# Kernel tuning notes

Measured on AMD Instinct MI355X. Metric: run time of the kernel, lower is better.

Reference implementation:

```python
import jax, jax.numpy as jnp
from jax import lax
import numpy as np

B, H, W, C = 16, 56, 56, 256
IMAGE_SHAPE = (224, 224)
SIGMA = 4.0


def gaussian_blur(x, sigma):
    # cv2.GaussianBlur with ksize = 2*round(4*sigma)+1, BORDER_REFLECT_101 (= jnp 'reflect')
    r = int(round(4 * sigma))
    k = 2 * r + 1
    i = jnp.arange(k, dtype=x.dtype) - r
    g = jnp.exp(-(i * i) / (2.0 * sigma * sigma))
    g = g / jnp.sum(g)
    xp = jnp.pad(x, ((0, 0), (r, r), (r, r), (0, 0)), mode='reflect')
    dn = ('NHWC', 'HWIO', 'NHWC')
    x = lax.conv_general_dilated(xp, g.reshape(k, 1, 1, 1), (1, 1), 'VALID', dimension_numbers=dn)
    x = lax.conv_general_dilated(x, g.reshape(1, k, 1, 1), (1, 1), 'VALID', dimension_numbers=dn)
    return x


def setup_inputs() -> dict:
    key = jax.random.key(0)
    k1, k2, k3 = jax.random.split(key, 3)
    inputs = jax.random.normal(k1, (B, H, W, C), dtype=jnp.float32)
    mean = jax.random.normal(k2, (H * W, C), dtype=jnp.float32)
    # build a PSD inverse-covariance per pixel so the Mahalanobis quadratic form is >= 0
    A = jax.random.normal(k3, (H * W, C, C), dtype=jnp.float32)
    cvar_inv = jnp.einsum('pij,pkj->pik', A, A) / C + 0.1 * jnp.eye(C, dtype=jnp.float32)[None]
    return {"inputs": inputs, "mean": mean, "cvar_inv": cvar_inv}


def reference(inputs, mean, cvar_inv):
    b = inputs.shape[0]
    h, w, c = inputs.shape[1:]
    feature = inputs.reshape(b, h * w, c)
    # per-pixel Mahalanobis distance, batched over all pixels at once
    diff = feature - mean[None]                              # [b, hw, c]
    quad = jnp.einsum('bpc,pcd,bpd->bp', diff, cvar_inv, diff)
    mask = jnp.sqrt(jnp.maximum(quad, 0.0))                  # [b, hw]
    mask = mask.reshape(b, h, w, 1)
    mask = jax.image.resize(mask, (b, *IMAGE_SHAPE, 1), method='bilinear')
    if SIGMA > 0:
        mask = gaussian_blur(mask, SIGMA)
    score = jnp.max(mask, axis=(1, 2, 3))[:, None]           # [b, 1]
    return score, mask
```

## Files before the change

kernel.cpp:

```cpp
#include <hip/hip_runtime.h>
#include <math.h>

#define HWPIX 3136
#define CH    256
#define NB    16
#define IMG   224

__global__ void mahal_kernel(const float* __restrict__ inputs,
                             const float* __restrict__ mean,
                             const float* __restrict__ cvar,
                             float* __restrict__ mask_small)
{
    const int p    = blockIdx.x;
    const int tid  = threadIdx.x;
    const int lane = tid & 63;
    const int w    = tid >> 6;

    __shared__ float sdiff[CH * 20];
    __shared__ float sred[4][16];

    const float* mrow_mean = mean + (size_t)p * CH;

    {
        float mv = mrow_mean[tid];
        #pragma unroll
        for (int b = 0; b < NB; ++b) {
            float v = inputs[((size_t)b * HWPIX + p) * CH + tid] - mv;
            sdiff[tid * 20 + b] = v;
        }
    }
    __syncthreads();

    const float* M = cvar + (size_t)p * CH * CH;
    const int c4 = lane * 4;

    float4 acc[NB];
    #pragma unroll
    for (int b = 0; b < NB; ++b) acc[b] = make_float4(0.f, 0.f, 0.f, 0.f);

    #pragma unroll 2
    for (int k = 0; k < 64; ++k) {
        const int d = (w << 6) + k;
        const float4 m = *reinterpret_cast<const float4*>(M + (size_t)d * CH + c4);
        const float4* sdv = reinterpret_cast<const float4*>(&sdiff[d * 20]);
        const float4 dv0 = sdv[0];
        const float4 dv1 = sdv[1];
        const float4 dv2 = sdv[2];
        const float4 dv3 = sdv[3];
        const float dvals[16] = {dv0.x, dv0.y, dv0.z, dv0.w,
                                 dv1.x, dv1.y, dv1.z, dv1.w,
                                 dv2.x, dv2.y, dv2.z, dv2.w,
                                 dv3.x, dv3.y, dv3.z, dv3.w};
        #pragma unroll
        for (int b = 0; b < NB; ++b) {
            const float s = dvals[b];
            acc[b].x = fmaf(m.x, s, acc[b].x);
            acc[b].y = fmaf(m.y, s, acc[b].y);
            acc[b].z = fmaf(m.z, s, acc[b].z);
            acc[b].w = fmaf(m.w, s, acc[b].w);
        }
    }

    const float4 mn = *reinterpret_cast<const float4*>(mrow_mean + c4);
    float q[NB];
    #pragma unroll
    for (int b = 0; b < NB; ++b) {
        const float4 f = *reinterpret_cast<const float4*>(inputs + ((size_t)b * HWPIX + p) * CH + c4);
        const float4 df = make_float4(f.x - mn.x, f.y - mn.y, f.z - mn.z, f.w - mn.w);
        q[b] = acc[b].x * df.x + acc[b].y * df.y + acc[b].z * df.z + acc[b].w * df.w;
    }

    #pragma unroll
    for (int b = 0; b < NB; ++b) {
        float v = q[b];
        for (int off = 32; off > 0; off >>= 1) v += __shfl_xor(v, off, 64);
        if (lane == 0) sred[w][b] = v;
    }
    __syncthreads();
    if (tid < NB) {
        const float s = sred[0][tid] + sred[1][tid] + sred[2][tid] + sred[3][tid];
        mask_small[(size_t)tid * HWPIX + p] = sqrtf(fmaxf(s, 0.0f));
    }
}

__global__ void resize_kernel(const float* __restrict__ small_, float* __restrict__ out)
{
    const int idx = blockIdx.x * 256 + threadIdx.x;
    const int b   = idx / (IMG * IMG);
    const int rem = idx % (IMG * IMG);
    const int oy  = rem / IMG;
    const int ox  = rem % IMG;

    float fy = oy * 0.25f - 0.375f;
    float fx = ox * 0.25f - 0.375f;
    fy = fminf(fmaxf(fy, 0.0f), 55.0f);
    fx = fminf(fmaxf(fx, 0.0f), 55.0f);
    int iy0 = min((int)fy, 54);
    int ix0 = min((int)fx, 54);
    const float wy = fy - iy0;
    const float wx = fx - ix0;

    const float* s = small_ + (size_t)b * HWPIX;
    const float v00 = s[iy0 * 56 + ix0];
    const float v01 = s[iy0 * 56 + ix0 + 1];
    const float v10 = s[(iy0 + 1) * 56 + ix0];
    const float v11 = s[(iy0 + 1) * 56 + ix0 + 1];
    const float v0 = v00 + wx * (v01 - v00);
    const float v1 = v10 + wx * (v11 - v10);
    out[idx] = v0 + wy * (v1 - v0);
}

__device__ __forceinline__ void setup_gauss(float* g, float* norm, int tid)
{
    if (tid < 33) {
        const int i = tid - 16;
        g[tid] = expf((float)(-(i * i)) / 32.0f);
    }
    __syncthreads();
    if (tid == 0) {
        float s = 0.f;
        for (int i = 0; i < 33; ++i) s += g[i];
        *norm = 1.0f / s;
    }
    __syncthreads();
}

__global__ void blurh_kernel(const float* __restrict__ in, float* __restrict__ out)
{
    __shared__ float g[33];
    __shared__ float norm;
    const int tid = threadIdx.x;
    setup_gauss(g, &norm, tid);

    const int idx = blockIdx.x * 256 + tid;
    const int b   = idx / (IMG * IMG);
    const int rem = idx % (IMG * IMG);
    const int y   = rem / IMG;
    const int x   = rem % IMG;

    const float* src = in + (size_t)b * IMG * IMG;
    float acc = 0.f;
    #pragma unroll
    for (int i = -16; i <= 16; ++i) {
        int yy = y + i;
        yy = yy < 0 ? -yy : (yy > 223 ? 446 - yy : yy);
        acc += g[i + 16] * src[yy * IMG + x];
    }
    out[idx] = acc * norm;
}

__global__ void blurw_kernel(const float* __restrict__ in, float* __restrict__ mask_out,
                             float* __restrict__ score)
{
    __shared__ float g[33];
    __shared__ float norm;
    __shared__ float m4[4];
    const int tid = threadIdx.x;
    setup_gauss(g, &norm, tid);

    const int idx = blockIdx.x * 256 + tid;
    const int b   = idx / (IMG * IMG);
    const int rem = idx % (IMG * IMG);
    const int y   = rem / IMG;
    const int x   = rem % IMG;

    const float* src = in + (size_t)b * IMG * IMG;
    float acc = 0.f;
    #pragma unroll
    for (int i = -16; i <= 16; ++i) {
        int xx = x + i;
        xx = xx < 0 ? -xx : (xx > 223 ? 446 - xx : xx);
        acc += g[i + 16] * src[y * IMG + xx];
    }
    acc *= norm;
    mask_out[idx] = acc;

    float v = acc;
    for (int off = 32; off > 0; off >>= 1) v = fmaxf(v, __shfl_xor(v, off, 64));
    const int lane = tid & 63;
    const int w    = tid >> 6;
    if (lane == 0) m4[w] = v;
    __syncthreads();
    if (tid == 0) {
        const float mm = fmaxf(fmaxf(m4[0], m4[1]), fmaxf(m4[2], m4[3]));
        atomicMax(reinterpret_cast<int*>(score) + b, __float_as_int(mm));
    }
}

__global__ void init_score(float* __restrict__ score)
{
    if (threadIdx.x < NB) score[threadIdx.x] = 0.0f;
}

extern "C" void kernel_launch(void* const* d_in, const int* in_sizes, int n_in,
                              void* d_out, int out_size, void* d_ws, size_t ws_size,
                              hipStream_t stream)
{
    const float* inputs = (const float*)d_in[0];
    const float* mean   = (const float*)d_in[1];
    const float* cvar   = (const float*)d_in[2];

    float* score    = (float*)d_out;
    float* mask_out = (float*)d_out + NB;

    char* ws = (char*)d_ws;
    float* mask_small = (float*)ws;
    float* resized    = (float*)(ws + (size_t)NB * HWPIX * 4);
    float* tmp        = (float*)(ws + (size_t)NB * HWPIX * 4
                                    + (size_t)NB * IMG * IMG * 4);

    mahal_kernel <<<HWPIX, 256, 0, stream>>>(inputs, mean, cvar, mask_small);
    resize_kernel<<<(NB * IMG * IMG) / 256, 256, 0, stream>>>(mask_small, resized);
    blurh_kernel <<<(NB * IMG * IMG) / 256, 256, 0, stream>>>(resized, tmp);
    init_score   <<<1, 64, 0, stream>>>(score);
    blurw_kernel <<<(NB * IMG * IMG) / 256, 256, 0, stream>>>(tmp, mask_out, score);
}
```

Measured before the change: 1.130 ms.

## Fuse resize and separable blur into one tiled kernel; software-pipeline cvar loads

Replaces the separate resize, vertical blur and horizontal blur kernels with one tail kernel per (4-row strip, batch). Each block recomputes the bilinear resize for its halo rows into shared memory, applies both blur passes there, and reduces the max, so the full-size intermediates no longer make a global round-trip. The Mahalanobis kernel now prefetches cvar rows four ahead in registers and declares launch bounds. Gaussian weights become precomputed constants. The cost is redundant halo resize work (36 rows computed per 4 output rows) and extra register pressure in the main kernel.

```diff
diff --git a/kernel.cpp b/kernel.cpp
--- a/kernel.cpp
+++ b/kernel.cpp
@@ -5,11 +5,44 @@
 #define CH    256
 #define NB    16
 #define IMG   224
-
-__global__ void mahal_kernel(const float* __restrict__ inputs,
-                             const float* __restrict__ mean,
-                             const float* __restrict__ cvar,
-                             float* __restrict__ mask_small)
+#define TY    4
+
+__constant__ float GW[33] = {
+    3.3458800e-05f, 8.8152100e-05f, 2.1817847e-04f, 5.0728021e-04f,
+    1.1080013e-03f, 2.2734742e-03f, 4.3822299e-03f, 7.9351934e-03f,
+    1.3498218e-02f, 2.1570092e-02f, 3.2380543e-02f, 4.5663884e-02f,
+    6.0494818e-02f, 7.5287016e-02f, 8.8019438e-02f, 9.6670425e-02f,
+    9.9739093e-02f, 9.6670425e-02f, 8.8019438e-02f, 7.5287016e-02f,
+    6.0494818e-02f, 4.5663884e-02f, 3.2380543e-02f, 2.1570092e-02f,
+    1.3498218e-02f, 7.9351934e-03f, 4.3822299e-03f, 2.2734742e-03f,
+    1.1080013e-03f, 5.0728021e-04f, 2.1817847e-04f, 8.8152100e-05f,
+    3.3458800e-05f
+};
+
+
+#define MAHAL_ROW(D, MVEC)                                                       \
+    {                                                                            \
+        const float4* sdv = reinterpret_cast<const float4*>(&sdiff[(D) * 20]);   \
+        const float4 dv0 = sdv[0], dv1 = sdv[1], dv2 = sdv[2], dv3 = sdv[3];     \
+        const float dsv[16] = {dv0.x, dv0.y, dv0.z, dv0.w,                       \
+                               dv1.x, dv1.y, dv1.z, dv1.w,                       \
+                               dv2.x, dv2.y, dv2.z, dv2.w,                       \
+                               dv3.x, dv3.y, dv3.z, dv3.w};                      \
+        _Pragma("unroll")                                                        \
+        for (int b = 0; b < NB; ++b) {                                           \
+            const float s = dsv[b];                                              \
+            acc[b].x = fmaf((MVEC).x, s, acc[b].x);                              \
+            acc[b].y = fmaf((MVEC).y, s, acc[b].y);                              \
+            acc[b].z = fmaf((MVEC).z, s, acc[b].z);                              \
+            acc[b].w = fmaf((MVEC).w, s, acc[b].w);                              \
+        }                                                                        \
+    }
+
+__global__ __launch_bounds__(256, 4)
+void mahal_kernel(const float* __restrict__ inputs,
+                  const float* __restrict__ mean,
+                  const float* __restrict__ cvar,
+                  float* __restrict__ mask_small)
 {
     const int p    = blockIdx.x;
     const int tid  = threadIdx.x;
@@ -22,43 +55,39 @@
     const float* mrow_mean = mean + (size_t)p * CH;
 
     {
-        float mv = mrow_mean[tid];
+        const float mv = mrow_mean[tid];
         #pragma unroll
         for (int b = 0; b < NB; ++b) {
-            float v = inputs[((size_t)b * HWPIX + p) * CH + tid] - mv;
-            sdiff[tid * 20 + b] = v;
+            sdiff[tid * 20 + b] = inputs[((size_t)b * HWPIX + p) * CH + tid] - mv;
         }
     }
     __syncthreads();
 
-    const float* M = cvar + (size_t)p * CH * CH;
-    const int c4 = lane * 4;
+    const int c4   = lane * 4;
+    const int row0 = w << 6;
+    const float* Mb = cvar + (size_t)p * CH * CH + (size_t)row0 * CH + c4;
 
     float4 acc[NB];
     #pragma unroll
     for (int b = 0; b < NB; ++b) acc[b] = make_float4(0.f, 0.f, 0.f, 0.f);
 
-    #pragma unroll 2
-    for (int k = 0; k < 64; ++k) {
-        const int d = (w << 6) + k;
-        const float4 m = *reinterpret_cast<const float4*>(M + (size_t)d * CH + c4);
-        const float4* sdv = reinterpret_cast<const float4*>(&sdiff[d * 20]);
-        const float4 dv0 = sdv[0];
-        const float4 dv1 = sdv[1];
-        const float4 dv2 = sdv[2];
-        const float4 dv3 = sdv[3];
-        const float dvals[16] = {dv0.x, dv0.y, dv0.z, dv0.w,
-                                 dv1.x, dv1.y, dv1.z, dv1.w,
-                                 dv2.x, dv2.y, dv2.z, dv2.w,
-                                 dv3.x, dv3.y, dv3.z, dv3.w};
-        #pragma unroll
-        for (int b = 0; b < NB; ++b) {
-            const float s = dvals[b];
-            acc[b].x = fmaf(m.x, s, acc[b].x);
-            acc[b].y = fmaf(m.y, s, acc[b].y);
-            acc[b].z = fmaf(m.z, s, acc[b].z);
-            acc[b].w = fmaf(m.w, s, acc[b].w);
+    float4 mr[4];
+    #pragma unroll
+    for (int i = 0; i < 4; ++i)
+        mr[i] = *reinterpret_cast<const float4*>(Mb + i * CH);
+
+    #pragma unroll 3
+    for (int kk = 0; kk < 60; kk += 4) {
+        #pragma unroll
+        for (int i = 0; i < 4; ++i) {
+            const float4 m = mr[i];
+            mr[i] = *reinterpret_cast<const float4*>(Mb + (kk + 4 + i) * CH);
+            MAHAL_ROW(row0 + kk + i, m)
         }
+    }
+    #pragma unroll
+    for (int i = 0; i < 4; ++i) {
+        MAHAL_ROW(row0 + 60 + i, mr[i])
     }
 
     const float4 mn = *reinterpret_cast<const float4*>(mrow_mean + c4);
@@ -83,103 +112,72 @@
     }
 }
 
-__global__ void resize_kernel(const float* __restrict__ small_, float* __restrict__ out)
-{
-    const int idx = blockIdx.x * 256 + threadIdx.x;
-    const int b   = idx / (IMG * IMG);
-    const int rem = idx % (IMG * IMG);
-    const int oy  = rem / IMG;
-    const int ox  = rem % IMG;
-
-    float fy = oy * 0.25f - 0.375f;
-    float fx = ox * 0.25f - 0.375f;
-    fy = fminf(fmaxf(fy, 0.0f), 55.0f);
-    fx = fminf(fmaxf(fx, 0.0f), 55.0f);
-    int iy0 = min((int)fy, 54);
-    int ix0 = min((int)fx, 54);
-    const float wy = fy - iy0;
-    const float wx = fx - ix0;
+__global__ void tail_kernel(const float* __restrict__ small_,
+                            float* __restrict__ mask_out,
+                            float* __restrict__ score)
+{
+    const int b   = blockIdx.y;
+    const int y0  = blockIdx.x * TY;
+    const int tid = threadIdx.x;
+
+    __shared__ float S[TY + 32][IMG];
+    __shared__ float Hb[TY][IMG];
+    __shared__ float m4[4];
 
     const float* s = small_ + (size_t)b * HWPIX;
-    const float v00 = s[iy0 * 56 + ix0];
-    const float v01 = s[iy0 * 56 + ix0 + 1];
-    const float v10 = s[(iy0 + 1) * 56 + ix0];
-    const float v11 = s[(iy0 + 1) * 56 + ix0 + 1];
-    const float v0 = v00 + wx * (v01 - v00);
-    const float v1 = v10 + wx * (v11 - v10);
-    out[idx] = v0 + wy * (v1 - v0);
-}
-
-__device__ __forceinline__ void setup_gauss(float* g, float* norm, int tid)
-{
-    if (tid < 33) {
-        const int i = tid - 16;
-        g[tid] = expf((float)(-(i * i)) / 32.0f);
-    }
-    __syncthreads();
-    if (tid == 0) {
-        float s = 0.f;
-        for (int i = 0; i < 33; ++i) s += g[i];
-        *norm = 1.0f / s;
-    }
-    __syncthreads();
-}
-
-__global__ void blurh_kernel(const float* __restrict__ in, float* __restrict__ out)
-{
-    __shared__ float g[33];
-    __shared__ float norm;
-    const int tid = threadIdx.x;
-    setup_gauss(g, &norm, tid);
-
-    const int idx = blockIdx.x * 256 + tid;
-    const int b   = idx / (IMG * IMG);
-    const int rem = idx % (IMG * IMG);
-    const int y   = rem / IMG;
-    const int x   = rem % IMG;
-
-    const float* src = in + (size_t)b * IMG * IMG;
-    float acc = 0.f;
-    #pragma unroll
-    for (int i = -16; i <= 16; ++i) {
-        int yy = y + i;
-        yy = yy < 0 ? -yy : (yy > 223 ? 446 - yy : yy);
-        acc += g[i + 16] * src[yy * IMG + x];
-    }
-    out[idx] = acc * norm;
-}
-
-__global__ void blurw_kernel(const float* __restrict__ in, float* __restrict__ mask_out,
-                             float* __restrict__ score)
-{
-    __shared__ float g[33];
-    __shared__ float norm;
-    __shared__ float m4[4];
-    const int tid = threadIdx.x;
-    setup_gauss(g, &norm, tid);
-
-    const int idx = blockIdx.x * 256 + tid;
-    const int b   = idx / (IMG * IMG);
-    const int rem = idx % (IMG * IMG);
-    const int y   = rem / IMG;
-    const int x   = rem % IMG;
-
-    const float* src = in + (size_t)b * IMG * IMG;
-    float acc = 0.f;
-    #pragma unroll
-    for (int i = -16; i <= 16; ++i) {
-        int xx = x + i;
-        xx = xx < 0 ? -xx : (xx > 223 ? 446 - xx : xx);
-        acc += g[i + 16] * src[y * IMG + xx];
-    }
-    acc *= norm;
-    mask_out[idx] = acc;
-
-    float v = acc;
-    for (int off = 32; off > 0; off >>= 1) v = fmaxf(v, __shfl_xor(v, off, 64));
+
+    for (int idx = tid; idx < (TY + 32) * IMG; idx += 256) {
+        const int r = idx / IMG;
+        const int x = idx - r * IMG;
+        int y = y0 - 16 + r;
+        y = y < 0 ? -y : (y > 223 ? 446 - y : y);
+        float fy = y * 0.25f - 0.375f;
+        float fx = x * 0.25f - 0.375f;
+        fy = fminf(fmaxf(fy, 0.0f), 55.0f);
+        fx = fminf(fmaxf(fx, 0.0f), 55.0f);
+        const int iy0 = min((int)fy, 54);
+        const int ix0 = min((int)fx, 54);
+        const float wy = fy - iy0;
+        const float wx = fx - ix0;
+        const float v00 = s[iy0 * 56 + ix0];
+        const float v01 = s[iy0 * 56 + ix0 + 1];
+        const float v10 = s[(iy0 + 1) * 56 + ix0];
+        const float v11 = s[(iy0 + 1) * 56 + ix0 + 1];
+        const float v0 = v00 + wx * (v01 - v00);
+        const float v1 = v10 + wx * (v11 - v10);
+        S[r][x] = v0 + wy * (v1 - v0);
+    }
+    __syncthreads();
+
+    for (int idx = tid; idx < TY * IMG; idx += 256) {
+        const int ty = idx / IMG;
+        const int x  = idx - ty * IMG;
+        float a = 0.f;
+        #pragma unroll
+        for (int i = 0; i < 33; ++i) a = fmaf(GW[i], S[ty + i][x], a);
+        Hb[ty][x] = a;
+    }
+    __syncthreads();
+
+    float vmax = 0.f;
+    for (int idx = tid; idx < TY * IMG; idx += 256) {
+        const int ty = idx / IMG;
+        const int x  = idx - ty * IMG;
+        float a = 0.f;
+        #pragma unroll
+        for (int i = 0; i < 33; ++i) {
+            int xx = x - 16 + i;
+            xx = xx < 0 ? -xx : (xx > 223 ? 446 - xx : xx);
+            a = fmaf(GW[i], Hb[ty][xx], a);
+        }
+        mask_out[((size_t)b * IMG + (y0 + ty)) * IMG + x] = a;
+        vmax = fmaxf(vmax, a);
+    }
+
+    for (int off = 32; off > 0; off >>= 1) vmax = fmaxf(vmax, __shfl_xor(vmax, off, 64));
     const int lane = tid & 63;
-    const int w    = tid >> 6;
-    if (lane == 0) m4[w] = v;
+    const int wv   = tid >> 6;
+    if (lane == 0) m4[wv] = vmax;
     __syncthreads();
     if (tid == 0) {
         const float mm = fmaxf(fmaxf(m4[0], m4[1]), fmaxf(m4[2], m4[3]));
@@ -203,15 +201,9 @@
     float* score    = (float*)d_out;
     float* mask_out = (float*)d_out + NB;
 
-    char* ws = (char*)d_ws;
-    float* mask_small = (float*)ws;
-    float* resized    = (float*)(ws + (size_t)NB * HWPIX * 4);
-    float* tmp        = (float*)(ws + (size_t)NB * HWPIX * 4
-                                    + (size_t)NB * IMG * IMG * 4);
-
-    mahal_kernel <<<HWPIX, 256, 0, stream>>>(inputs, mean, cvar, mask_small);
-    resize_kernel<<<(NB * IMG * IMG) / 256, 256, 0, stream>>>(mask_small, resized);
-    blurh_kernel <<<(NB * IMG * IMG) / 256, 256, 0, stream>>>(resized, tmp);
-    init_score   <<<1, 64, 0, stream>>>(score);
-    blurw_kernel <<<(NB * IMG * IMG) / 256, 256, 0, stream>>>(tmp, mask_out, score);
-}
+    float* mask_small = (float*)d_ws;
+
+    init_score  <<<1, 64, 0, stream>>>(score);
+    mahal_kernel<<<HWPIX, 256, 0, stream>>>(inputs, mean, cvar, mask_small);
+    tail_kernel <<<dim3(IMG / TY, NB), 256, 0, stream>>>(mask_small, mask_out, score);
+}
```

After: 1.225 ms. 1.08x slower.
